# Performance work log

Hardware: AMD Instinct MI355X
Metric: run time of the kernel (lower is better)

Reference implementation:

```python
import jax, jax.numpy as jnp
import numpy as np

GROUPS = 32
GN_EPS = 1e-6


def setup_inputs() -> dict:
    key = jax.random.key(0)
    ks = jax.random.split(key, 6)
    B, C, H, W = 2, 512, 64, 64
    s = 1.0 / np.sqrt(C)
    return {
        "x": jax.random.normal(ks[0], (B, C, H, W), jnp.float32),
        "gamma": jnp.ones((C,), jnp.float32),
        "beta": jnp.zeros((C,), jnp.float32),
        "wq": jax.random.normal(ks[1], (C, C), jnp.float32) * s,
        "bq": jnp.zeros((C,), jnp.float32),
        "wk": jax.random.normal(ks[2], (C, C), jnp.float32) * s,
        "bk": jnp.zeros((C,), jnp.float32),
        "wv": jax.random.normal(ks[3], (C, C), jnp.float32) * s,
        "bv": jnp.zeros((C,), jnp.float32),
        "wp": jax.random.normal(ks[4], (C, C), jnp.float32) * s,
        "bp": jnp.zeros((C,), jnp.float32),
    }


def _group_norm(x, gamma, beta):
    B, C, H, W = x.shape
    xg = x.reshape(B, GROUPS, C // GROUPS, H, W)
    mean = jnp.mean(xg, axis=(2, 3, 4), keepdims=True)
    var = jnp.mean(jnp.square(xg - mean), axis=(2, 3, 4), keepdims=True)
    xn = ((xg - mean) * jax.lax.rsqrt(var + GN_EPS)).reshape(B, C, H, W)
    return xn * gamma[None, :, None, None] + beta[None, :, None, None]


def _conv1x1(x, w, b):
    # 1x1 conv == per-pixel linear over channels; w: [out, in]
    return jnp.einsum('oc,bchw->bohw', w, x) + b[None, :, None, None]


def reference(x, gamma, beta, wq, bq, wk, bk, wv, bv, wp, bp):
    B, C, H, W = x.shape
    N = H * W
    h = _group_norm(x, gamma, beta)
    q = _conv1x1(h, wq, bq).reshape(B, C, N)  # [B, C, N]
    k = _conv1x1(h, wk, bk).reshape(B, C, N)
    v = _conv1x1(h, wv, bv).reshape(B, C, N)
    scale = C ** (-0.5)
    # attn[b, i, j] = softmax_j(q_i . k_j * scale)
    scores = jnp.einsum('bci,bcj->bij', q, k) * scale
    attn = jax.nn.softmax(scores, axis=2)
    # out[b, c, i] = sum_j attn[b, i, j] * v[b, c, j]
    o = jnp.einsum('bij,bcj->bci', attn, v).reshape(B, C, H, W)
    o = _conv1x1(o, wp, bp)
    return x + o
```

## Files before the change

### kernel.cpp

```cpp
#include <hip/hip_runtime.h>
#include <hip/hip_bf16.h>

using bf16 = __hip_bfloat16;
typedef __attribute__((ext_vector_type(4))) float f32x4;
typedef __attribute__((ext_vector_type(8))) short bf16x8;

#define NPX 4096
#define CCH 512

struct Ptr4 { void* p0; void* p1; void* p2; void* p3; };

__device__ __forceinline__ void async16(const bf16* g, bf16* l) {
  __builtin_amdgcn_global_load_lds((const __attribute__((address_space(1))) void*)g,
                                   (__attribute__((address_space(3))) void*)l, 16, 0, 0);
}

__device__ __forceinline__ float bfb2f(short s) {
  unsigned u = ((unsigned)(unsigned short)s) << 16;
  float f;
  __builtin_memcpy(&f, &u, 4);
  return f;
}

__device__ __forceinline__ short f2bfb(float f) {
  bf16 h = __float2bfloat16(f);
  short s;
  __builtin_memcpy(&s, &h, 2);
  return s;
}

__device__ __forceinline__ void xcd_swz(unsigned& bx, unsigned& by, unsigned& bz) {
  unsigned nx = gridDim.x, ny = gridDim.y;
  unsigned flat = (blockIdx.z * ny + blockIdx.y) * nx + blockIdx.x;
  unsigned nwg = nx * ny * gridDim.z;
  unsigned swz = (flat & 7) * (nwg >> 3) + (flat >> 3);
  bx = swz % nx;
  unsigned tmp = swz / nx;
  by = tmp % ny;
  bz = tmp / ny;
}

__global__ __launch_bounds__(256) void convert_weights_kernel(
    const float* __restrict__ wq, const float* __restrict__ wk,
    const float* __restrict__ wv, const float* __restrict__ wp,
    const float* __restrict__ bq, const float* __restrict__ bk,
    bf16* __restrict__ wout, float* __restrict__ bqk, float* __restrict__ rowsum) {
  int tid = blockIdx.x * 256 + threadIdx.x;
  int i = tid * 4;
  int seg = i >> 18;
  const float* in = seg == 0 ? wq : seg == 1 ? wk : seg == 2 ? wv : wp;
  float4 v = *reinterpret_cast<const float4*>(in + (i & 262143));
  wout[i]     = __float2bfloat16(v.x);
  wout[i + 1] = __float2bfloat16(v.y);
  wout[i + 2] = __float2bfloat16(v.z);
  wout[i + 3] = __float2bfloat16(v.w);
  if (tid < 256) {
    int j = tid * 4;
    const float* bsrc = j < 512 ? bq : bk;
    float4 b = *reinterpret_cast<const float4*>(bsrc + (j & 511));
    *reinterpret_cast<float4*>(bqk + j) = b;
  }
  if (tid < 2048) {
    float4 z = {0.f, 0.f, 0.f, 0.f};
    *reinterpret_cast<float4*>(rowsum + tid * 4) = z;
  }
}

__global__ __launch_bounds__(256) void gn_stats_kernel(const float* __restrict__ x,
                                                       float* __restrict__ stats) {
  const float* p = x + (size_t)blockIdx.x * 65536;
  float s = 0.f, s2 = 0.f;
  int t = threadIdx.x;
  for (int i = t * 4; i < 65536; i += 256 * 4) {
    float4 v = *reinterpret_cast<const float4*>(p + i);
    s  += v.x + v.y + v.z + v.w;
    s2 += v.x * v.x + v.y * v.y + v.z * v.z + v.w * v.w;
  }
  #pragma unroll
  for (int off = 32; off >= 1; off >>= 1) {
    s  += __shfl_xor(s, off);
    s2 += __shfl_xor(s2, off);
  }
  __shared__ float ls[8];
  int wv = t >> 6;
  if ((t & 63) == 0) { ls[wv * 2] = s; ls[wv * 2 + 1] = s2; }
  __syncthreads();
  if (t == 0) {
    float S  = ls[0] + ls[2] + ls[4] + ls[6];
    float S2 = ls[1] + ls[3] + ls[5] + ls[7];
    float mean = S * (1.f / 65536.f);
    float var  = S2 * (1.f / 65536.f) - mean * mean;
    stats[blockIdx.x * 2]     = mean;
    stats[blockIdx.x * 2 + 1] = rsqrtf(var + 1e-6f);
  }
}

__global__ __launch_bounds__(256) void gn_apply_kernel(const float* __restrict__ x,
    const float* __restrict__ stats, const float* __restrict__ gamma,
    const float* __restrict__ beta, bf16* __restrict__ h) {
  __shared__ float tile[64][65];
  int b  = blockIdx.z;
  int c0 = blockIdx.x * 64, n0 = blockIdx.y * 64;
  int t  = threadIdx.x;
  int cl = t >> 6, nl = t & 63;
  #pragma unroll
  for (int i = 0; i < 16; i++) {
    int c = c0 + cl + i * 4;
    float v = x[((size_t)b * CCH + c) * NPX + n0 + nl];
    int g = c >> 4;
    float mean = stats[(b * 32 + g) * 2];
    float rstd = stats[(b * 32 + g) * 2 + 1];
    tile[cl + i * 4][nl] = (v - mean) * rstd * gamma[c] + beta[c];
  }
  __syncthreads();
  #pragma unroll
  for (int i = 0; i < 16; i++) {
    int n = cl + i * 4;
    int c = nl;
    h[((size_t)b * NPX + n0 + n) * CCH + c0 + c] = __float2bfloat16(tile[c][n]);
  }
}

template<int OMODE>
__global__ __launch_bounds__(256, 2) void gemm_bt_kernel(
    const bf16* __restrict__ A, const bf16* __restrict__ B, void* __restrict__ C,
    const float* __restrict__ bias_m, const float* __restrict__ bias_n,
    const float* __restrict__ resid, float* __restrict__ rowsum, float alpha, int K,
    int lda, int ldb, int ldc,
    long long sA, long long sB, long long sC, long long sR) {
  unsigned bxi, byi, bz;
  xcd_swz(bxi, byi, bz);
  A += (size_t)bz * sA;
  B += (size_t)bz * sB;
  const int m0 = bxi * 128, n0 = byi * 128;

  __shared__ bf16 ldsA[128 * 64];
  __shared__ bf16 ldsB[128 * 64];

  const int t = threadIdx.x;
  const int lane = t & 63, wv = t >> 6;
  const int wr = (wv >> 1) * 64, wc = (wv & 1) * 64;

  const int r0 = t >> 3;
  const int cb = ((t & 7) << 4) ^ ((r0 & 7) << 4);
  const bf16* gA = A + (size_t)(m0 + r0) * lda + (cb >> 1);
  const bf16* gB = B + (size_t)(n0 + r0) * ldb + (cb >> 1);
  bf16* lA = ldsA + t * 8;
  bf16* lB = ldsB + t * 8;

  const int arow = wr + (lane & 15);
  const int brow = wc + (lane & 15);
  const int kb   = (lane >> 4) * 16;

  f32x4 acc[4][4] = {};

  for (int k0 = 0; k0 < K; k0 += 64) {
    #pragma unroll
    for (int i = 0; i < 4; i++) {
      async16(gA + (size_t)i * 32 * lda + k0, lA + i * 2048);
      async16(gB + (size_t)i * 32 * ldb + k0, lB + i * 2048);
    }
    __syncthreads();
    #pragma unroll
    for (int ks = 0; ks < 2; ks++) {
      bf16x8 af[4], bfr[4];
      #pragma unroll
      for (int f = 0; f < 4; f++) {
        int ra = arow + f * 16;
        af[f] = *reinterpret_cast<const bf16x8*>(
            reinterpret_cast<const char*>(ldsA) + ra * 128 + ((ks * 64 + kb) ^ ((ra & 7) << 4)));
        int rb = brow + f * 16;
        bfr[f] = *reinterpret_cast<const bf16x8*>(
            reinterpret_cast<const char*>(ldsB) + rb * 128 + ((ks * 64 + kb) ^ ((rb & 7) << 4)));
      }
      #pragma unroll
      for (int fm = 0; fm < 4; fm++)
        #pragma unroll
        for (int fn = 0; fn < 4; fn++)
          acc[fm][fn] = __builtin_amdgcn_mfma_f32_16x16x32_bf16(af[fm], bfr[fn], acc[fm][fn], 0, 0, 0);
    }
    __syncthreads();
  }

  #pragma unroll
  for (int fm = 0; fm < 4; fm++) {
    #pragma unroll
    for (int j = 0; j < 4; j++) {
      int gm = m0 + wr + fm * 16 + (lane >> 4) * 4 + j;
      if (OMODE == 2) {
        float rsum = 0.f;
        #pragma unroll
        for (int fn = 0; fn < 4; fn++) {
          int gn = n0 + wc + fn * 16 + (lane & 15);
          float e = __expf(acc[fm][fn][j] * alpha);
          rsum += e;
          reinterpret_cast<bf16*>(C)[(size_t)bz * sC + (size_t)gm * ldc + gn] = __float2bfloat16(e);
        }
        rsum += __shfl_xor(rsum, 1);
        rsum += __shfl_xor(rsum, 2);
        rsum += __shfl_xor(rsum, 4);
        rsum += __shfl_xor(rsum, 8);
        if ((lane & 15) == 0) atomicAdd(rowsum + bz * 4096 + gm, rsum);
      } else {
        float bm = bias_m ? bias_m[gm] : 0.f;
        #pragma unroll
        for (int fn = 0; fn < 4; fn++) {
          int gn = n0 + wc + fn * 16 + (lane & 15);
          float vv = acc[fm][fn][j] * alpha + bm;
          if (bias_n) vv += bias_n[gn];
          if (resid)  vv += resid[(size_t)bz * sR + (size_t)gm * ldc + gn];
          if (OMODE == 1)
            reinterpret_cast<bf16*>(C)[(size_t)bz * sC + (size_t)gm * ldc + gn] = __float2bfloat16(vv);
          else
            reinterpret_cast<float*>(C)[(size_t)bz * sC + (size_t)gm * ldc + gn] = vv;
        }
      }
    }
  }
}

__global__ __launch_bounds__(256, 2) void pv_split_kernel(
    const bf16* __restrict__ Sb, const bf16* __restrict__ vb,
    const float* __restrict__ rowsum,
    long long sS, long long sV, Ptr4 slots, int split_only) {
  unsigned bxi, byi, bz;
  xcd_swz(bxi, byi, bz);
  const int z = bz;
  const int b = split_only ? 0 : (z >> 1);
  const int s = split_only ? z : (z & 1);
  const bf16* A = Sb + (size_t)b * sS + s * 2048;
  const bf16* B = vb + (size_t)b * sV + s * 2048;
  const float* rs = rowsum + b * 4096;
  bf16* Cp = (bf16*)((&slots.p0)[z]);
  const int m0 = bxi * 128, n0 = byi * 128;

  __shared__ bf16 ldsA[128 * 64];
  __shared__ bf16 ldsB[128 * 64];

  const int t = threadIdx.x;
  const int lane = t & 63, wv = t >> 6;
  const int wr = (wv >> 1) * 64, wc = (wv & 1) * 64;

  const int r0 = t >> 3;
  const int cb = ((t & 7) << 4) ^ ((r0 & 7) << 4);
  const bf16* gA = A + (size_t)(m0 + r0) * 4096 + (cb >> 1);
  const bf16* gB = B + (size_t)(n0 + r0) * 4096 + (cb >> 1);
  bf16* lA = ldsA + t * 8;
  bf16* lB = ldsB + t * 8;

  const int arow = wr + (lane & 15);
  const int brow = wc + (lane & 15);
  const int kb   = (lane >> 4) * 16;

  f32x4 acc[4][4] = {};

  for (int k0 = 0; k0 < 2048; k0 += 64) {
    #pragma unroll
    for (int i = 0; i < 4; i++) {
      async16(gA + (size_t)i * 32 * 4096 + k0, lA + i * 2048);
      async16(gB + (size_t)i * 32 * 4096 + k0, lB + i * 2048);
    }
    __syncthreads();
    #pragma unroll
    for (int ks = 0; ks < 2; ks++) {
      bf16x8 af[4], bfr[4];
      #pragma unroll
      for (int f = 0; f < 4; f++) {
        int ra = arow + f * 16;
        af[f] = *reinterpret_cast<const bf16x8*>(
            reinterpret_cast<const char*>(ldsA) + ra * 128 + ((ks * 64 + kb) ^ ((ra & 7) << 4)));
        int rb = brow + f * 16;
        bfr[f] = *reinterpret_cast<const bf16x8*>(
            reinterpret_cast<const char*>(ldsB) + rb * 128 + ((ks * 64 + kb) ^ ((rb & 7) << 4)));
      }
      #pragma unroll
      for (int fm = 0; fm < 4; fm++)
        #pragma unroll
        for (int fn = 0; fn < 4; fn++)
          acc[fm][fn] = __builtin_amdgcn_mfma_f32_16x16x32_bf16(af[fm], bfr[fn], acc[fm][fn], 0, 0, 0);
    }
    __syncthreads();
  }

  #pragma unroll
  for (int fm = 0; fm < 4; fm++) {
    #pragma unroll
    for (int j = 0; j < 4; j++) {
      int gm = m0 + wr + fm * 16 + (lane >> 4) * 4 + j;
      float inv = 1.0f / rs[gm];
      #pragma unroll
      for (int fn = 0; fn < 4; fn++) {
        int gn = n0 + wc + fn * 16 + (lane & 15);
        Cp[(size_t)gm * 512 + gn] = __float2bfloat16(acc[fm][fn][j] * inv);
      }
    }
  }
}

__global__ __launch_bounds__(256) void reduce_add_kernel(bf16* __restrict__ dst,
                                                         const bf16* __restrict__ src, int n) {
  int i = (blockIdx.x * 256 + threadIdx.x) * 8;
  if (i + 7 < n) {
    bf16x8 a = *reinterpret_cast<const bf16x8*>(dst + i);
    bf16x8 b = *reinterpret_cast<const bf16x8*>(src + i);
    bf16x8 r;
    #pragma unroll
    for (int j = 0; j < 8; j++) r[j] = f2bfb(bfb2f(a[j]) + bfb2f(b[j]));
    *reinterpret_cast<bf16x8*>(dst + i) = r;
  }
}

extern "C" void kernel_launch(void* const* d_in, const int* in_sizes, int n_in,
                              void* d_out, int out_size, void* d_ws, size_t ws_size,
                              hipStream_t stream) {
  const float* x     = (const float*)d_in[0];
  const float* gamma = (const float*)d_in[1];
  const float* beta  = (const float*)d_in[2];
  const float* wq    = (const float*)d_in[3];
  const float* bq    = (const float*)d_in[4];
  const float* wk    = (const float*)d_in[5];
  const float* bk    = (const float*)d_in[6];
  const float* wv    = (const float*)d_in[7];
  const float* bv    = (const float*)d_in[8];
  const float* wp    = (const float*)d_in[9];
  const float* bp    = (const float*)d_in[10];
  float* out = (float*)d_out;

  char* w = (char*)d_ws;
  size_t off = 0;
  float* stats  = (float*)(w + off);   off += 4096;
  float* bqk    = (float*)(w + off);   off += 4096;
  float* rowsum = (float*)(w + off);   off += 32768;
  bf16* wqkb = (bf16*)(w + off);       off += (size_t)1024 * 512 * 2;
  bf16* wvb  = (bf16*)(w + off);       off += (size_t)512 * 512 * 2;
  bf16* wpb  = (bf16*)(w + off);       off += (size_t)512 * 512 * 2;
  bf16* h    = (bf16*)(w + off);       off += (size_t)2 * NPX * CCH * 2;
  bf16* qk   = (bf16*)(w + off);       off += (size_t)2 * NPX * 1024 * 2;
  bf16* v    = (bf16*)(w + off);       off += (size_t)2 * NPX * CCH * 2;
  bf16* o    = (bf16*)(w + off);       off += (size_t)2 * NPX * CCH * 2;
  bf16* S    = (bf16*)(w + off);
  size_t need_big = off + (size_t)2 * NPX * NPX * 2;
  const bool big = ws_size >= need_big;

  const long long sBN = (long long)NPX * CCH;
  const long long sQK = (long long)NPX * 1024;
  const long long sS  = (long long)NPX * NPX;
  const float scale = 0.04419417382415922f;

  convert_weights_kernel<<<1024, 256, 0, stream>>>(wq, wk, wv, wp, bq, bk, wqkb, bqk, rowsum);
  gn_stats_kernel<<<64, 256, 0, stream>>>(x, stats);
  gn_apply_kernel<<<dim3(8, 64, 2), 256, 0, stream>>>(x, stats, gamma, beta, h);

  gemm_bt_kernel<1><<<dim3(32, 8, 2), 256, 0, stream>>>(h, wqkb, qk, nullptr, bqk, nullptr,
      nullptr, 1.f, 512, 512, 512, 1024, sBN, 0, sQK, 0);
  gemm_bt_kernel<1><<<dim3(4, 32, 2), 256, 0, stream>>>(wvb, h, v, bv, nullptr, nullptr,
      nullptr, 1.f, 512, 512, 512, 4096, 0, sBN, sBN, 0);

  if (big) {
    gemm_bt_kernel<2><<<dim3(32, 32, 2), 256, 0, stream>>>(qk, qk + 512, S,
        nullptr, nullptr, nullptr, rowsum, scale, 512, 1024, 1024, 4096, sQK, sQK, sS, 0);
    Ptr4 slots{h, o, qk, o + sBN};
    pv_split_kernel<<<dim3(32, 4, 4), 256, 0, stream>>>(S, v, rowsum, sS, sBN, slots, 0);
    reduce_add_kernel<<<1024, 256, 0, stream>>>(o, h, NPX * CCH);
    reduce_add_kernel<<<1024, 256, 0, stream>>>(o + sBN, qk, NPX * CCH);
  } else {
    for (int b = 0; b < 2; b++) {
      gemm_bt_kernel<2><<<dim3(32, 32, 1), 256, 0, stream>>>(qk + b * sQK, qk + b * sQK + 512, S,
          nullptr, nullptr, nullptr, rowsum + b * 4096, scale, 512, 1024, 1024, 4096, 0, 0, 0, 0);
      Ptr4 slots{h, o + b * sBN, h, h};
      pv_split_kernel<<<dim3(32, 4, 2), 256, 0, stream>>>(S, v + b * sBN, rowsum + b * 4096,
          0, 0, slots, 1);
      reduce_add_kernel<<<1024, 256, 0, stream>>>(o + b * sBN, h, NPX * CCH);
    }
  }

  gemm_bt_kernel<0><<<dim3(4, 32, 2), 256, 0, stream>>>(wpb, o, out, bp, nullptr, x,
      nullptr, 1.f, 512, 512, 512, 4096, 0, sBN, sBN, sBN);
}
```

Baseline: 286.7 us.

## Merge launches, replace rowsum atomics with partial sums, raise occupancy

Folds weight conversion and GroupNorm partial statistics into one prep kernel, and spreads the stats over more blocks (8 per group) so gn_apply finishes the reduction. Q/K and V projections now run in one launch through a runtime-parameterised GEMM that picks its problem per block. Softmax row sums are written as per-tile partials instead of atomics and reduced in the PV kernel's prologue, and the two reduce-adds are merged into one launch. Launch bounds go from 2 to 4 waves per SIMD, which cuts launch count and atomic contention but risks register spilling, and the output mode becomes a runtime branch.

Measured after the change: 273.9 us. 4.5% less time.

```diff
diff --git a/kernel.cpp b/kernel.cpp
--- a/kernel.cpp
+++ b/kernel.cpp
@@ -9,6 +9,17 @@
 #define CCH 512
 
 struct Ptr4 { void* p0; void* p1; void* p2; void* p3; };
+
+struct GemmP {
+  const bf16* A; const bf16* B; void* C;
+  const float* bias_m; const float* bias_n; const float* resid;
+  float* rspart;
+  float alpha; int K;
+  int lda, ldb, ldc;
+  long long sA, sB, sC, sR;
+  int gx, gy;
+  int omode;
+};
 
 __device__ __forceinline__ void async16(const bf16* g, bf16* l) {
   __builtin_amdgcn_global_load_lds((const __attribute__((address_space(1))) void*)g,
@@ -29,88 +40,85 @@
   return s;
 }
 
-__device__ __forceinline__ void xcd_swz(unsigned& bx, unsigned& by, unsigned& bz) {
-  unsigned nx = gridDim.x, ny = gridDim.y;
-  unsigned flat = (blockIdx.z * ny + blockIdx.y) * nx + blockIdx.x;
-  unsigned nwg = nx * ny * gridDim.z;
-  unsigned swz = (flat & 7) * (nwg >> 3) + (flat >> 3);
-  bx = swz % nx;
-  unsigned tmp = swz / nx;
-  by = tmp % ny;
-  bz = tmp / ny;
-}
-
-__global__ __launch_bounds__(256) void convert_weights_kernel(
+__global__ __launch_bounds__(256) void prep_kernel(
     const float* __restrict__ wq, const float* __restrict__ wk,
     const float* __restrict__ wv, const float* __restrict__ wp,
     const float* __restrict__ bq, const float* __restrict__ bk,
-    bf16* __restrict__ wout, float* __restrict__ bqk, float* __restrict__ rowsum) {
-  int tid = blockIdx.x * 256 + threadIdx.x;
-  int i = tid * 4;
-  int seg = i >> 18;
-  const float* in = seg == 0 ? wq : seg == 1 ? wk : seg == 2 ? wv : wp;
-  float4 v = *reinterpret_cast<const float4*>(in + (i & 262143));
-  wout[i]     = __float2bfloat16(v.x);
-  wout[i + 1] = __float2bfloat16(v.y);
-  wout[i + 2] = __float2bfloat16(v.z);
-  wout[i + 3] = __float2bfloat16(v.w);
-  if (tid < 256) {
-    int j = tid * 4;
-    const float* bsrc = j < 512 ? bq : bk;
-    float4 b = *reinterpret_cast<const float4*>(bsrc + (j & 511));
-    *reinterpret_cast<float4*>(bqk + j) = b;
-  }
-  if (tid < 2048) {
-    float4 z = {0.f, 0.f, 0.f, 0.f};
-    *reinterpret_cast<float4*>(rowsum + tid * 4) = z;
-  }
-}
-
-__global__ __launch_bounds__(256) void gn_stats_kernel(const float* __restrict__ x,
-                                                       float* __restrict__ stats) {
-  const float* p = x + (size_t)blockIdx.x * 65536;
-  float s = 0.f, s2 = 0.f;
+    const float* __restrict__ x,
+    bf16* __restrict__ wout, float* __restrict__ bqk, float* __restrict__ pstats) {
+  int bid = blockIdx.x;
   int t = threadIdx.x;
-  for (int i = t * 4; i < 65536; i += 256 * 4) {
-    float4 v = *reinterpret_cast<const float4*>(p + i);
-    s  += v.x + v.y + v.z + v.w;
-    s2 += v.x * v.x + v.y * v.y + v.z * v.z + v.w * v.w;
-  }
-  #pragma unroll
-  for (int off = 32; off >= 1; off >>= 1) {
-    s  += __shfl_xor(s, off);
-    s2 += __shfl_xor(s2, off);
-  }
-  __shared__ float ls[8];
-  int wv = t >> 6;
-  if ((t & 63) == 0) { ls[wv * 2] = s; ls[wv * 2 + 1] = s2; }
-  __syncthreads();
-  if (t == 0) {
-    float S  = ls[0] + ls[2] + ls[4] + ls[6];
-    float S2 = ls[1] + ls[3] + ls[5] + ls[7];
-    float mean = S * (1.f / 65536.f);
-    float var  = S2 * (1.f / 65536.f) - mean * mean;
-    stats[blockIdx.x * 2]     = mean;
-    stats[blockIdx.x * 2 + 1] = rsqrtf(var + 1e-6f);
+  if (bid < 1024) {
+    int tid = bid * 256 + t;
+    int i = tid * 4;
+    int seg = i >> 18;
+    const float* in = seg == 0 ? wq : seg == 1 ? wk : seg == 2 ? wv : wp;
+    float4 v = *reinterpret_cast<const float4*>(in + (i & 262143));
+    wout[i]     = __float2bfloat16(v.x);
+    wout[i + 1] = __float2bfloat16(v.y);
+    wout[i + 2] = __float2bfloat16(v.z);
+    wout[i + 3] = __float2bfloat16(v.w);
+    if (tid < 256) {
+      int j = tid * 4;
+      const float* bsrc = j < 512 ? bq : bk;
+      float4 b = *reinterpret_cast<const float4*>(bsrc + (j & 511));
+      *reinterpret_cast<float4*>(bqk + j) = b;
+    }
+  } else {
+    int bp = bid - 1024;
+    const float* p = x + (size_t)bp * 8192;
+    float s = 0.f, s2 = 0.f;
+    #pragma unroll
+    for (int j = 0; j < 8; j++) {
+      float4 v = *reinterpret_cast<const float4*>(p + j * 1024 + t * 4);
+      s  += v.x + v.y + v.z + v.w;
+      s2 += v.x * v.x + v.y * v.y + v.z * v.z + v.w * v.w;
+    }
+    #pragma unroll
+    for (int off = 32; off >= 1; off >>= 1) {
+      s  += __shfl_xor(s, off);
+      s2 += __shfl_xor(s2, off);
+    }
+    __shared__ float ls[8];
+    int wv_ = t >> 6;
+    if ((t & 63) == 0) { ls[wv_ * 2] = s; ls[wv_ * 2 + 1] = s2; }
+    __syncthreads();
+    if (t == 0) {
+      pstats[bp * 2]     = ls[0] + ls[2] + ls[4] + ls[6];
+      pstats[bp * 2 + 1] = ls[1] + ls[3] + ls[5] + ls[7];
+    }
   }
 }
 
 __global__ __launch_bounds__(256) void gn_apply_kernel(const float* __restrict__ x,
-    const float* __restrict__ stats, const float* __restrict__ gamma,
+    const float* __restrict__ pstats, const float* __restrict__ gamma,
     const float* __restrict__ beta, bf16* __restrict__ h) {
   __shared__ float tile[64][65];
+  __shared__ float mr[4][2];
   int b  = blockIdx.z;
   int c0 = blockIdx.x * 64, n0 = blockIdx.y * 64;
   int t  = threadIdx.x;
+  if (t < 4) {
+    int g = (c0 >> 4) + t;
+    float S = 0.f, S2 = 0.f;
+    #pragma unroll
+    for (int k2 = 0; k2 < 8; k2++) {
+      S  += pstats[((b * 32 + g) * 8 + k2) * 2];
+      S2 += pstats[((b * 32 + g) * 8 + k2) * 2 + 1];
+    }
+    float mean = S * (1.f / 65536.f);
+    float var  = S2 * (1.f / 65536.f) - mean * mean;
+    mr[t][0] = mean;
+    mr[t][1] = rsqrtf(var + 1e-6f);
+  }
+  __syncthreads();
   int cl = t >> 6, nl = t & 63;
   #pragma unroll
   for (int i = 0; i < 16; i++) {
     int c = c0 + cl + i * 4;
     float v = x[((size_t)b * CCH + c) * NPX + n0 + nl];
-    int g = c >> 4;
-    float mean = stats[(b * 32 + g) * 2];
-    float rstd = stats[(b * 32 + g) * 2 + 1];
-    tile[cl + i * 4][nl] = (v - mean) * rstd * gamma[c] + beta[c];
+    int gi = (cl + i * 4) >> 4;
+    tile[cl + i * 4][nl] = (v - mr[gi][0]) * mr[gi][1] * gamma[c] + beta[c];
   }
   __syncthreads();
   #pragma unroll
@@ -121,17 +129,19 @@
   }
 }
 
-template<int OMODE>
-__global__ __launch_bounds__(256, 2) void gemm_bt_kernel(
-    const bf16* __restrict__ A, const bf16* __restrict__ B, void* __restrict__ C,
-    const float* __restrict__ bias_m, const float* __restrict__ bias_n,
-    const float* __restrict__ resid, float* __restrict__ rowsum, float alpha, int K,
-    int lda, int ldb, int ldc,
-    long long sA, long long sB, long long sC, long long sR) {
-  unsigned bxi, byi, bz;
-  xcd_swz(bxi, byi, bz);
-  A += (size_t)bz * sA;
-  B += (size_t)bz * sB;
+__global__ __launch_bounds__(256, 4) void gemm_any_kernel(GemmP p0, GemmP p1, unsigned nb0) {
+  unsigned nwg = gridDim.x;
+  unsigned flat = blockIdx.x;
+  unsigned swz = (flat & 7) * (nwg >> 3) + (flat >> 3);
+  GemmP p = swz < nb0 ? p0 : p1;
+  unsigned local = swz < nb0 ? swz : swz - nb0;
+  unsigned bxi = local % p.gx;
+  unsigned tmp = local / p.gx;
+  unsigned byi = tmp % p.gy;
+  unsigned bz  = tmp / p.gy;
+
+  const bf16* A = p.A + (size_t)bz * p.sA;
+  const bf16* B = p.B + (size_t)bz * p.sB;
   const int m0 = bxi * 128, n0 = byi * 128;
 
   __shared__ bf16 ldsA[128 * 64];
@@ -143,8 +153,8 @@
 
   const int r0 = t >> 3;
   const int cb = ((t & 7) << 4) ^ ((r0 & 7) << 4);
-  const bf16* gA = A + (size_t)(m0 + r0) * lda + (cb >> 1);
-  const bf16* gB = B + (size_t)(n0 + r0) * ldb + (cb >> 1);
+  const bf16* gA = A + (size_t)(m0 + r0) * p.lda + (cb >> 1);
+  const bf16* gB = B + (size_t)(n0 + r0) * p.ldb + (cb >> 1);
   bf16* lA = ldsA + t * 8;
   bf16* lB = ldsB + t * 8;
 
@@ -154,11 +164,11 @@
 
   f32x4 acc[4][4] = {};
 
-  for (int k0 = 0; k0 < K; k0 += 64) {
+  for (int k0 = 0; k0 < p.K; k0 += 64) {
     #pragma unroll
     for (int i = 0; i < 4; i++) {
-      async16(gA + (size_t)i * 32 * lda + k0, lA + i * 2048);
-      async16(gB + (size_t)i * 32 * ldb + k0, lB + i * 2048);
+      async16(gA + (size_t)i * 32 * p.lda + k0, lA + i * 2048);
+      async16(gB + (size_t)i * 32 * p.ldb + k0, lB + i * 2048);
     }
     __syncthreads();
     #pragma unroll
@@ -187,57 +197,77 @@
     #pragma unroll
     for (int j = 0; j < 4; j++) {
       int gm = m0 + wr + fm * 16 + (lane >> 4) * 4 + j;
-      if (OMODE == 2) {
+      if (p.omode == 2) {
         float rsum = 0.f;
         #pragma unroll
         for (int fn = 0; fn < 4; fn++) {
           int gn = n0 + wc + fn * 16 + (lane & 15);
-          float e = __expf(acc[fm][fn][j] * alpha);
+          float e = __expf(acc[fm][fn][j] * p.alpha);
           rsum += e;
-          reinterpret_cast<bf16*>(C)[(size_t)bz * sC + (size_t)gm * ldc + gn] = __float2bfloat16(e);
+          reinterpret_cast<bf16*>(p.C)[(size_t)bz * p.sC + (size_t)gm * p.ldc + gn] = __float2bfloat16(e);
         }
         rsum += __shfl_xor(rsum, 1);
         rsum += __shfl_xor(rsum, 2);
         rsum += __shfl_xor(rsum, 4);
         rsum += __shfl_xor(rsum, 8);
-        if ((lane & 15) == 0) atomicAdd(rowsum + bz * 4096 + gm, rsum);
+        if ((lane & 15) == 0)
+          p.rspart[(((size_t)bz * 4096 + gm) << 6) + byi * 2 + (wv & 1)] = rsum;
       } else {
-        float bm = bias_m ? bias_m[gm] : 0.f;
+        float bm = p.bias_m ? p.bias_m[gm] : 0.f;
         #pragma unroll
         for (int fn = 0; fn < 4; fn++) {
           int gn = n0 + wc + fn * 16 + (lane & 15);
-          float vv = acc[fm][fn][j] * alpha + bm;
-          if (bias_n) vv += bias_n[gn];
-          if (resid)  vv += resid[(size_t)bz * sR + (size_t)gm * ldc + gn];
-          if (OMODE == 1)
-            reinterpret_cast<bf16*>(C)[(size_t)bz * sC + (size_t)gm * ldc + gn] = __float2bfloat16(vv);
+          float vv = acc[fm][fn][j] * p.alpha + bm;
+          if (p.bias_n) vv += p.bias_n[gn];
+          if (p.resid)  vv += p.resid[(size_t)bz * p.sR + (size_t)gm * p.ldc + gn];
+          if (p.omode == 1)
+            reinterpret_cast<bf16*>(p.C)[(size_t)bz * p.sC + (size_t)gm * p.ldc + gn] = __float2bfloat16(vv);
           else
-            reinterpret_cast<float*>(C)[(size_t)bz * sC + (size_t)gm * ldc + gn] = vv;
+            reinterpret_cast<float*>(p.C)[(size_t)bz * p.sC + (size_t)gm * p.ldc + gn] = vv;
         }
       }
     }
   }
 }
 
-__global__ __launch_bounds__(256, 2) void pv_split_kernel(
+__global__ __launch_bounds__(256, 4) void pv_split_kernel(
     const bf16* __restrict__ Sb, const bf16* __restrict__ vb,
-    const float* __restrict__ rowsum,
+    const float* __restrict__ rspart,
     long long sS, long long sV, Ptr4 slots, int split_only) {
-  unsigned bxi, byi, bz;
-  xcd_swz(bxi, byi, bz);
+  unsigned nx = gridDim.x, ny = gridDim.y;
+  unsigned flat = (blockIdx.z * ny + blockIdx.y) * nx + blockIdx.x;
+  unsigned nwg = nx * ny * gridDim.z;
+  unsigned swz = (flat & 7) * (nwg >> 3) + (flat >> 3);
+  unsigned bxi = swz % nx;
+  unsigned tmp = swz / nx;
+  unsigned byi = tmp % ny;
+  unsigned bz  = tmp / ny;
+
   const int z = bz;
   const int b = split_only ? 0 : (z >> 1);
   const int s = split_only ? z : (z & 1);
   const bf16* A = Sb + (size_t)b * sS + s * 2048;
   const bf16* B = vb + (size_t)b * sV + s * 2048;
-  const float* rs = rowsum + b * 4096;
   bf16* Cp = (bf16*)((&slots.p0)[z]);
   const int m0 = bxi * 128, n0 = byi * 128;
 
   __shared__ bf16 ldsA[128 * 64];
   __shared__ bf16 ldsB[128 * 64];
+  __shared__ float rs_lds[128];
 
   const int t = threadIdx.x;
+
+  if (t < 128) {
+    const float4* pp = reinterpret_cast<const float4*>(rspart + (((size_t)b * 4096 + m0 + t) << 6));
+    float ssum = 0.f;
+    #pragma unroll
+    for (int i2 = 0; i2 < 16; i2++) {
+      float4 vv = pp[i2];
+      ssum += vv.x + vv.y + vv.z + vv.w;
+    }
+    rs_lds[t] = 1.0f / ssum;
+  }
+
   const int lane = t & 63, wv = t >> 6;
   const int wr = (wv >> 1) * 64, wc = (wv & 1) * 64;
 
@@ -286,8 +316,9 @@
   for (int fm = 0; fm < 4; fm++) {
     #pragma unroll
     for (int j = 0; j < 4; j++) {
-      int gm = m0 + wr + fm * 16 + (lane >> 4) * 4 + j;
-      float inv = 1.0f / rs[gm];
+      int lrow = wr + fm * 16 + (lane >> 4) * 4 + j;
+      float inv = rs_lds[lrow];
+      int gm = m0 + lrow;
       #pragma unroll
       for (int fn = 0; fn < 4; fn++) {
         int gn = n0 + wc + fn * 16 + (lane & 15);
@@ -295,6 +326,18 @@
       }
     }
   }
+}
+
+__global__ __launch_bounds__(256) void reduce_add2_kernel(bf16* __restrict__ o,
+    const bf16* __restrict__ hsrc, const bf16* __restrict__ qksrc) {
+  int i = (blockIdx.x * 256 + threadIdx.x) * 8;
+  const bf16* src = i < 2097152 ? hsrc + i : qksrc + (i - 2097152);
+  bf16x8 a = *reinterpret_cast<const bf16x8*>(o + i);
+  bf16x8 b = *reinterpret_cast<const bf16x8*>(src);
+  bf16x8 r;
+  #pragma unroll
+  for (int j = 0; j < 8; j++) r[j] = f2bfb(bfb2f(a[j]) + bfb2f(b[j]));
+  *reinterpret_cast<bf16x8*>(o + i) = r;
 }
 
 __global__ __launch_bounds__(256) void reduce_add_kernel(bf16* __restrict__ dst,
@@ -328,9 +371,9 @@
 
   char* w = (char*)d_ws;
   size_t off = 0;
-  float* stats  = (float*)(w + off);   off += 4096;
+  float* pstats = (float*)(w + off);   off += 4096;
   float* bqk    = (float*)(w + off);   off += 4096;
-  float* rowsum = (float*)(w + off);   off += 32768;
+  float* rspart = (float*)(w + off);   off += (size_t)2 * 4096 * 64 * 4;
   bf16* wqkb = (bf16*)(w + off);       off += (size_t)1024 * 512 * 2;
   bf16* wvb  = (bf16*)(w + off);       off += (size_t)512 * 512 * 2;
   bf16* wpb  = (bf16*)(w + off);       off += (size_t)512 * 512 * 2;
@@ -347,33 +390,36 @@
   const long long sS  = (long long)NPX * NPX;
   const float scale = 0.04419417382415922f;
 
-  convert_weights_kernel<<<1024, 256, 0, stream>>>(wq, wk, wv, wp, bq, bk, wqkb, bqk, rowsum);
-  gn_stats_kernel<<<64, 256, 0, stream>>>(x, stats);
-  gn_apply_kernel<<<dim3(8, 64, 2), 256, 0, stream>>>(x, stats, gamma, beta, h);
-
-  gemm_bt_kernel<1><<<dim3(32, 8, 2), 256, 0, stream>>>(h, wqkb, qk, nullptr, bqk, nullptr,
-      nullptr, 1.f, 512, 512, 512, 1024, sBN, 0, sQK, 0);
-  gemm_bt_kernel<1><<<dim3(4, 32, 2), 256, 0, stream>>>(wvb, h, v, bv, nullptr, nullptr,
-      nullptr, 1.f, 512, 512, 512, 4096, 0, sBN, sBN, 0);
+  prep_kernel<<<1536, 256, 0, stream>>>(wq, wk, wv, wp, bq, bk, x, wqkb, bqk, pstats);
+  gn_apply_kernel<<<dim3(8, 64, 2), 256, 0, stream>>>(x, pstats, gamma, beta, h);
+
+  GemmP pqkv = {h, wqkb, qk, nullptr, bqk, nullptr, nullptr,
+                1.f, 512, 512, 512, 1024, sBN, 0, sQK, 0, 32, 8, 1};
+  GemmP pv   = {wvb, h, v, bv, nullptr, nullptr, nullptr,
+                1.f, 512, 512, 512, 4096, 0, sBN, sBN, 0, 4, 32, 1};
+  gemm_any_kernel<<<768, 256, 0, stream>>>(pqkv, pv, 512);
 
   if (big) {
-    gemm_bt_kernel<2><<<dim3(32, 32, 2), 256, 0, stream>>>(qk, qk + 512, S,
-        nullptr, nullptr, nullptr, rowsum, scale, 512, 1024, 1024, 4096, sQK, sQK, sS, 0);
+    GemmP ps = {qk, qk + 512, S, nullptr, nullptr, nullptr, rspart,
+                scale, 512, 1024, 1024, 4096, sQK, sQK, sS, 0, 32, 32, 2};
+    gemm_any_kernel<<<2048, 256, 0, stream>>>(ps, ps, 2048);
     Ptr4 slots{h, o, qk, o + sBN};
-    pv_split_kernel<<<dim3(32, 4, 4), 256, 0, stream>>>(S, v, rowsum, sS, sBN, slots, 0);
-    reduce_add_kernel<<<1024, 256, 0, stream>>>(o, h, NPX * CCH);
-    reduce_add_kernel<<<1024, 256, 0, stream>>>(o + sBN, qk, NPX * CCH);
+    pv_split_kernel<<<dim3(32, 4, 4), 256, 0, stream>>>(S, v, rspart, sS, sBN, slots, 0);
+    reduce_add2_kernel<<<2048, 256, 0, stream>>>(o, h, qk);
   } else {
     for (int b = 0; b < 2; b++) {
-      gemm_bt_kernel<2><<<dim3(32, 32, 1), 256, 0, stream>>>(qk + b * sQK, qk + b * sQK + 512, S,
-          nullptr, nullptr, nullptr, rowsum + b * 4096, scale, 512, 1024, 1024, 4096, 0, 0, 0, 0);
+      GemmP ps = {qk + b * sQK, qk + b * sQK + 512, S, nullptr, nullptr, nullptr,
+                  rspart + ((size_t)b << 18),
+                  scale, 512, 1024, 1024, 4096, 0, 0, 0, 0, 32, 32, 2};
+      gemm_any_kernel<<<1024, 256, 0, stream>>>(ps, ps, 1024);
       Ptr4 slots{h, o + b * sBN, h, h};
-      pv_split_kernel<<<dim3(32, 4, 2), 256, 0, stream>>>(S, v + b * sBN, rowsum + b * 4096,
-          0, 0, slots, 1);
-      reduce_add_kernel<<<1024, 256, 0, stream>>>(o + b * sBN, h, NPX * CCH);
-    }
-  }
-
-  gemm_bt_kernel<0><<<dim3(4, 32, 2), 256, 0, stream>>>(wpb, o, out, bp, nullptr, x,
-      nullptr, 1.f, 512, 512, 512, 4096, 0, sBN, sBN, sBN);
-}
+      pv_split_kernel<<<dim3(32, 4, 2), 256, 0, stream>>>(S, v + b * sBN,
+          rspart + ((size_t)b << 18), 0, 0, slots, 1);
+      reduce_add_kernel<<<1024, 256, 0, stream>>>(o + b * sBN, h, 2097152);
+    }
+  }
+
+  GemmP po = {wpb, o, out, bp, nullptr, x, nullptr,
+              1.f, 512, 512, 512, 4096, 0, sBN, sBN, sBN, 4, 32, 0};
+  gemm_any_kernel<<<256, 256, 0, stream>>>(po, po, 256);
+}
```
